# Optimization experiments

Hardware: AMD Instinct MI355X
Metric: run time of the kernel (lower is better)

## Reference

```python
import jax, jax.numpy as jnp
import numpy as np
from jax.scipy.special import logsumexp

N = 8192       # number of vectors being quantized
E_DIM = 768    # embedding dim
N_E = 1024     # codebook size per layer
SK_EPS = (0.0, 0.003, 0.003, 0.003)
SK_ITERS = 100
BETA = 1.0


def setup_inputs() -> dict:
    key = jax.random.key(0)
    ks = jax.random.split(key, 5)
    inp = {"x": jax.random.normal(ks[0], (N, E_DIM), jnp.float32)}
    for i in range(4):
        inp[f"codebook_{i}"] = jax.random.normal(ks[i + 1], (N_E, E_DIM), jnp.float32) * 0.02
    return inp


def _sq_dist(x, e):
    # squared euclidean cdist: [N, K]
    return (jnp.sum(x * x, axis=1, keepdims=True)
            + jnp.sum(e * e, axis=1)[None, :]
            - 2.0 * (x @ e.T))


def _sinkhorn_indices(d, eps, iters):
    # log-domain Sinkhorn on Q = exp(-d/eps); constants (1/K, 1/B) dropped
    # since they do not affect the final argmax assignment.
    logQ = -d / eps  # [N, K]

    def body(_, lq):
        lq = lq - logsumexp(lq, axis=0, keepdims=True)  # normalize per code over batch
        lq = lq - logsumexp(lq, axis=1, keepdims=True)  # normalize per sample over codes
        return lq

    logQ = jax.lax.fori_loop(0, iters, body, logQ)
    return jnp.argmax(logQ, axis=1)


def _vq_layer(residual, codebook, eps):
    d = _sq_dist(residual, codebook)
    if eps > 0:
        indices = _sinkhorn_indices(d, eps, SK_ITERS)
    else:
        indices = jnp.argmin(d, axis=1)
    x_q = codebook[indices]  # gather [N, E_DIM]
    sg = jax.lax.stop_gradient
    loss = jnp.mean((sg(x_q) - residual) ** 2) + BETA * jnp.mean((x_q - sg(residual)) ** 2)
    x_q = residual + sg(x_q - residual)  # straight-through estimator
    return x_q, loss, indices


def reference(x, codebook_0, codebook_1, codebook_2, codebook_3):
    codebooks = (codebook_0, codebook_1, codebook_2, codebook_3)
    residual = x
    x_q = jnp.zeros_like(x)
    losses, all_idx = [], []
    for cb, eps in zip(codebooks, SK_EPS):
        xr, loss, idx = _vq_layer(residual, cb, eps)
        residual = residual - xr
        x_q = x_q + xr
        losses.append(loss)
        all_idx.append(idx)
    mean_loss = jnp.stack(losses).mean()
    indices = jnp.stack(all_idx, axis=-1)  # [N, num_quantizers]
    return x_q, mean_loss, indices
```

## Files before the change

kernel.cpp:

```cpp
#include <hip/hip_runtime.h>
#include <math.h>

#define N_VEC   8192
#define EDIM    768
#define NCODES  1024
#define SKITERS 100
#define ROWS_PB 32
#define CHUNKS  (N_VEC / ROWS_PB)
#define DYN_LDS ((32 * NCODES + 32) * 4)

__device__ __forceinline__ void ast(float* p, float v) {
  __hip_atomic_store(p, v, __ATOMIC_RELAXED, __HIP_MEMORY_SCOPE_AGENT);
}
__device__ __forceinline__ void asti(int* p, int v) {
  __hip_atomic_store(p, v, __ATOMIC_RELAXED, __HIP_MEMORY_SCOPE_AGENT);
}
__device__ __forceinline__ int aldi(int* p) {
  return __hip_atomic_load(p, __ATOMIC_RELAXED, __HIP_MEMORY_SCOPE_AGENT);
}
union MS { unsigned long long u; float2 f; };
__device__ __forceinline__ void astms(unsigned long long* p, float m, float s) {
  MS x; x.f.x = m; x.f.y = s;
  __hip_atomic_store(p, x.u, __ATOMIC_RELAXED, __HIP_MEMORY_SCOPE_AGENT);
}
__device__ __forceinline__ float2 aldms(unsigned long long* p) {
  MS x; x.u = __hip_atomic_load(p, __ATOMIC_RELAXED, __HIP_MEMORY_SCOPE_AGENT);
  return x.f;
}
union TV { unsigned long long u; struct { float v; unsigned g; } p; };
__device__ __forceinline__ TV tvload(const unsigned long long* p) {
  TV x; x.u = __hip_atomic_load((unsigned long long*)p, __ATOMIC_RELAXED, __HIP_MEMORY_SCOPE_AGENT);
  return x;
}
__device__ __forceinline__ void tvstore(unsigned long long* p, float v, unsigned g) {
  TV x; x.p.v = v; x.p.g = g;
  __hip_atomic_store(p, x.u, __ATOMIC_RELAXED, __HIP_MEMORY_SCOPE_AGENT);
}

__device__ __forceinline__ float np_base96_sq(const float* a) {
  float r[8];
#pragma unroll
  for (int j = 0; j < 8; ++j) r[j] = __fmul_rn(a[j], a[j]);
  for (int i = 8; i < 96; i += 8) {
#pragma unroll
    for (int j = 0; j < 8; ++j) r[j] = __fadd_rn(r[j], __fmul_rn(a[i + j], a[i + j]));
  }
  float c01 = __fadd_rn(r[0], r[1]);
  float c23 = __fadd_rn(r[2], r[3]);
  float c45 = __fadd_rn(r[4], r[5]);
  float c67 = __fadd_rn(r[6], r[7]);
  return __fadd_rn(__fadd_rn(c01, c23), __fadd_rn(c45, c67));
}
__device__ __forceinline__ float np_ssq768(const float* a) {
  float L[8];
#pragma unroll
  for (int t = 0; t < 8; ++t) L[t] = np_base96_sq(a + 96 * t);
  float a01 = __fadd_rn(L[0], L[1]);
  float a23 = __fadd_rn(L[2], L[3]);
  float a45 = __fadd_rn(L[4], L[5]);
  float a67 = __fadd_rn(L[6], L[7]);
  return __fadd_rn(__fadd_rn(a01, a23), __fadd_rn(a45, a67));
}

__global__ __launch_bounds__(64) void rows_ssq(const float* __restrict__ a,
                                               float* __restrict__ out, int nrows) {
  int row = blockIdx.x * 64 + threadIdx.x;
  if (row < nrows) out[row] = np_ssq768(a + (size_t)row * EDIM);
}

#define BM 128
#define BN 128
#define BK 16
template <bool LAYER0>
__global__ __launch_bounds__(256) void gemm_d(const float* __restrict__ A,
                                              const float* __restrict__ B,
                                              const float* __restrict__ sumrr,
                                              const float* __restrict__ sumee,
                                              float* __restrict__ V) {
  __shared__ float As[BK][BM];
  __shared__ float Bs[BK][BN];
  int tid = threadIdx.x;
  int bm = blockIdx.y * BM;
  int bn = blockIdx.x * BN;
  int lr = tid >> 1;
  int lc = (tid & 1) << 3;
  const float* Ap = A + (size_t)(bm + lr) * EDIM + lc;
  const float* Bp = B + (size_t)(bn + lr) * EDIM + lc;
  float acc[8][8];
#pragma unroll
  for (int i = 0; i < 8; ++i)
#pragma unroll
    for (int j = 0; j < 8; ++j) acc[i][j] = 0.f;
  int ty = tid >> 4, tx = tid & 15;
  for (int k0 = 0; k0 < EDIM; k0 += BK) {
    float4 a0 = *(const float4*)(Ap + k0);
    float4 a1 = *(const float4*)(Ap + k0 + 4);
    float4 b0 = *(const float4*)(Bp + k0);
    float4 b1 = *(const float4*)(Bp + k0 + 4);
    __syncthreads();
    As[lc + 0][lr] = a0.x; As[lc + 1][lr] = a0.y; As[lc + 2][lr] = a0.z; As[lc + 3][lr] = a0.w;
    As[lc + 4][lr] = a1.x; As[lc + 5][lr] = a1.y; As[lc + 6][lr] = a1.z; As[lc + 7][lr] = a1.w;
    Bs[lc + 0][lr] = b0.x; Bs[lc + 1][lr] = b0.y; Bs[lc + 2][lr] = b0.z; Bs[lc + 3][lr] = b0.w;
    Bs[lc + 4][lr] = b1.x; Bs[lc + 5][lr] = b1.y; Bs[lc + 6][lr] = b1.z; Bs[lc + 7][lr] = b1.w;
    __syncthreads();
#pragma unroll
    for (int k = 0; k < BK; ++k) {
      float av[8], bv[8];
      *(float4*)(av)     = *(const float4*)(&As[k][ty * 8]);
      *(float4*)(av + 4) = *(const float4*)(&As[k][ty * 8 + 4]);
      *(float4*)(bv)     = *(const float4*)(&Bs[k][tx * 8]);
      *(float4*)(bv + 4) = *(const float4*)(&Bs[k][tx * 8 + 4]);
#pragma unroll
      for (int i = 0; i < 8; ++i)
#pragma unroll
        for (int j = 0; j < 8; ++j) acc[i][j] = __fmaf_rn(av[i], bv[j], acc[i][j]);
    }
  }
#pragma unroll
  for (int i = 0; i < 8; ++i) {
    int row = bm + ty * 8 + i;
    float srr = sumrr[row];
    float* Vp = V + (size_t)row * NCODES + bn + tx * 8;
#pragma unroll
    for (int j = 0; j < 8; ++j) {
      int col = bn + tx * 8 + j;
      float s1 = __fadd_rn(srr, sumee[col]);
      float dv = __fsub_rn(s1, __fmul_rn(2.0f, acc[i][j]));
      Vp[j] = LAYER0 ? dv : __fdiv_rn(-dv, 0.003f);
    }
  }
}

__device__ __forceinline__ void accf(float w, float& m, float& s) {
  float d = __fsub_rn(w, m);
  float e = expf(-fabsf(d));
  bool gt = (w > m);
  s = gt ? __fadd_rn(__fmul_rn(s, e), 1.0f) : __fadd_rn(s, e);
  m = gt ? w : m;
}
__device__ __forceinline__ void mergef(float mo, float so, float& m, float& s) {
  float mn = fmaxf(m, mo);
  if (mn == -INFINITY) { s = 0.f; return; }
  float d = __fsub_rn(mo, m);
  float e = expf(-fabsf(d));
  bool gt = (mo > m);
  s = gt ? __fadd_rn(__fmul_rn(s, e), so) : __fadd_rn(s, __fmul_rn(so, e));
  m = mn;
}

__global__ __launch_bounds__(1024) void sk_persist(float* __restrict__ lq,
                                                   unsigned long long* __restrict__ part,
                                                   unsigned long long* __restrict__ cT,
                                                   int* __restrict__ parr,
                                                   int* __restrict__ xarr,
                                                   unsigned gen0) {
  extern __shared__ float lds[];
  float (*vL)[NCODES] = (float(*)[NCODES])lds;
  float* rowLs = lds + 32 * NCODES;
  int tid = threadIdx.x, b = blockIdx.x;
  int wave = tid >> 6, lane = tid & 63;
  int r0 = b * ROWS_PB;

  float v[32];
#pragma unroll
  for (int r = 0; r < 32; ++r) v[r] = lq[(size_t)(r0 + r) * NCODES + tid];

#define COLCHAIN_ARRIVE(GEN)                                                  \
  do {                                                                        \
    float m = -INFINITY, s = 0.f;                                             \
    _Pragma("unroll")                                                         \
    for (int r = 0; r < 32; ++r) accf(v[r], m, s);                            \
    astms(&part[(size_t)b * NCODES + tid], m, s);                             \
    asm volatile("s_waitcnt vmcnt(0)" ::: "memory");                          \
    __syncthreads();                                                          \
    if (tid == 0) asti(&parr[b * 16], (GEN));                                 \
  } while (0)

  COLCHAIN_ARRIVE(1);

  for (int t = 0; t < SKITERS; ++t) {
    int gen = t + 1;
    unsigned cg = gen0 + (unsigned)gen;

    if (wave == 0) {
      if (b < 8) {
        if (lane < 32) {
          int* fl = &parr[(b * 32 + lane) * 16];
          while (aldi(fl) < gen) __builtin_amdgcn_s_sleep(1);
        }
        asm volatile("" ::: "memory");
        if (lane == 0) asti(&xarr[b * 16], gen);
      }
      if (lane < 8) {
        int* fl = &xarr[lane * 16];
        while (aldi(fl) < gen) __builtin_amdgcn_s_sleep(1);
      }
      asm volatile("" ::: "memory");
      float m = -INFINITY, s = 0.f;
      if (lane < 32) {
        int colj = lane >> 3, grp = lane & 7;
        int col = 4 * b + colj;
#pragma unroll
        for (int qb = 0; qb < 32; qb += 16) {
          float2 pv[16];
#pragma unroll
          for (int q = 0; q < 16; ++q)
            pv[q] = aldms(&part[(size_t)(grp * 32 + qb + q) * NCODES + col]);
#pragma unroll
          for (int q = 0; q < 16; ++q) mergef(pv[q].x, pv[q].y, m, s);
        }
      }
      float mm = -INFINITY, ss = 0.f;
#pragma unroll
      for (int g2 = 0; g2 < 8; ++g2) {
        float mo = __shfl(m, ((lane & 3) << 3) + g2, 64);
        float so = __shfl(s, ((lane & 3) << 3) + g2, 64);
        mergef(mo, so, mm, ss);
      }
      if (lane < 4) tvstore(&cT[4 * b + lane], __fadd_rn(logf(ss), mm), cg);
    }

    float cl;
    {
      TV cv = tvload(&cT[tid]);
      while (cv.p.g < cg) { __builtin_amdgcn_s_sleep(1); cv = tvload(&cT[tid]); }
      cl = cv.p.v;
    }

#pragma unroll
    for (int r = 0; r < 32; ++r) {
      v[r] = __fsub_rn(v[r], cl);
      vL[r][tid] = v[r];
    }
    __syncthreads();

#pragma unroll
    for (int rr = 0; rr < 2; ++rr) {
      int row = wave * 2 + rr;
      float vals[16];
#pragma unroll
      for (int k = 0; k < 16; ++k) vals[k] = vL[row][lane + (k << 6)];
      float mx = vals[0];
#pragma unroll
      for (int k = 1; k < 16; ++k) mx = fmaxf(mx, vals[k]);
      for (int off = 32; off; off >>= 1) mx = fmaxf(mx, __shfl_xor(mx, off, 64));
      float s = 0.f;
#pragma unroll
      for (int k = 0; k < 16; ++k) s = __fadd_rn(s, expf(__fsub_rn(vals[k], mx)));
      for (int off = 32; off; off >>= 1) s = __fadd_rn(s, __shfl_xor(s, off, 64));
      if (lane == 0) rowLs[row] = __fadd_rn(logf(s), mx);
    }
    __syncthreads();
#pragma unroll
    for (int r = 0; r < 32; ++r) v[r] = __fsub_rn(v[r], rowLs[r]);

    if (t < SKITERS - 1) COLCHAIN_ARRIVE(gen + 1);
  }

#pragma unroll
  for (int r = 0; r < 32; ++r) lq[(size_t)(r0 + r) * NCODES + tid] = v[r];
#undef COLCHAIN_ARRIVE
}

template <int MODE>
__global__ __launch_bounds__(256) void epi(const float* __restrict__ V,
                                           const float* __restrict__ rin,
                                           const float* __restrict__ cb,
                                           float* __restrict__ rout,
                                           double* __restrict__ rowssq,
                                           float* __restrict__ idx_out,
                                           int layer) {
  int i = blockIdx.x;
  int tid = threadIdx.x;
  const float* Vrow = V + (size_t)i * NCODES;
  float bv = MODE ? -INFINITY : INFINITY;
  int bj = 0;
  for (int j = tid; j < NCODES; j += 256) {
    float v = Vrow[j];
    bool better = MODE ? (v > bv) : (v < bv);
    if (better) { bv = v; bj = j; }
  }
  __shared__ float sv[256];
  __shared__ int   sj[256];
  sv[tid] = bv; sj[tid] = bj;
  __syncthreads();
  for (int st = 128; st; st >>= 1) {
    if (tid < st) {
      float v2 = sv[tid + st]; int j2 = sj[tid + st];
      bool better = MODE ? (v2 > sv[tid]) : (v2 < sv[tid]);
      if (better || (v2 == sv[tid] && j2 < sj[tid])) { sv[tid] = v2; sj[tid] = j2; }
    }
    __syncthreads();
  }
  int idx = sj[0];
  const float* crow = cb + (size_t)idx * EDIM;
  double p = 0.0;
  for (int c = tid; c < EDIM; c += 256) {
    float rn = __fsub_rn(rin[(size_t)i * EDIM + c], crow[c]);
    rout[(size_t)i * EDIM + c] = rn;
    p += (double)rn * (double)rn;
  }
  for (int off = 32; off; off >>= 1) p += __shfl_xor(p, off, 64);
  __shared__ double wsum[4];
  if ((tid & 63) == 0) wsum[tid >> 6] = p;
  __syncthreads();
  if (tid == 0) {
    rowssq[i] = wsum[0] + wsum[1] + wsum[2] + wsum[3];
    idx_out[(size_t)i * 4 + layer] = (float)idx;
  }
}

__global__ __launch_bounds__(1024) void loss_final(const double* __restrict__ rowssq,
                                                   float* __restrict__ out_loss) {
  int tid = threadIdx.x;
  __shared__ double acc[16];
  __shared__ double ltot;
  if (tid == 0) ltot = 0.0;
  __syncthreads();
  for (int l = 0; l < 4; ++l) {
    double p = 0.0;
    for (int i = tid; i < N_VEC; i += 1024) p += rowssq[l * N_VEC + i];
    for (int off = 32; off; off >>= 1) p += __shfl_xor(p, off, 64);
    if ((tid & 63) == 0) acc[tid >> 6] = p;
    __syncthreads();
    if (tid == 0) {
      double sl = 0.0;
      for (int w = 0; w < 16; ++w) sl += acc[w];
      ltot += 2.0 * sl / ((double)N_VEC * (double)EDIM);
    }
    __syncthreads();
  }
  if (tid == 0) out_loss[0] = (float)(ltot * 0.25);
}

__global__ __launch_bounds__(256) void xq_final(const float* __restrict__ x,
                                                float* __restrict__ out) {
  size_t i = ((size_t)blockIdx.x * 256 + threadIdx.x) * 4;
  float4 xv = *(const float4*)(x + i);
  float4 rv = *(const float4*)(out + i);
  float4 o;
  o.x = __fsub_rn(xv.x, rv.x); o.y = __fsub_rn(xv.y, rv.y);
  o.z = __fsub_rn(xv.z, rv.z); o.w = __fsub_rn(xv.w, rv.w);
  *(float4*)(out + i) = o;
}

extern "C" void kernel_launch(void* const* d_in, const int* in_sizes, int n_in,
                              void* d_out, int out_size, void* d_ws, size_t ws_size,
                              hipStream_t stream) {
  const float* x = (const float*)d_in[0];
  const float* cbs[4] = {(const float*)d_in[1], (const float*)d_in[2],
                         (const float*)d_in[3], (const float*)d_in[4]};
  float* out = (float*)d_out;
  float* resid = out;
  float* loss_out = out + (size_t)N_VEC * EDIM;
  float* idx_out = loss_out + 1;

  float* ws = (float*)d_ws;
  float* lq = ws;
  unsigned long long* part = (unsigned long long*)(lq + (size_t)N_VEC * NCODES);
  unsigned long long* cT = part + (size_t)CHUNKS * NCODES;
  float* sumrr = (float*)(cT + NCODES);
  float* sumee = sumrr + N_VEC;
  double* rowssq = (double*)(sumee + 4 * NCODES);
  int* flagbase = (int*)(rowssq + 4 * N_VEC);

  static int lds_set = 0;
  if (!lds_set) {
    hipFuncSetAttribute((const void*)sk_persist,
                        hipFuncAttributeMaxDynamicSharedMemorySize, DYN_LDS);
    lds_set = 1;
  }

  hipMemsetAsync(cT, 0, NCODES * 8, stream);
  hipMemsetAsync(flagbase, 0, 4 * 8192 * sizeof(int), stream);

  for (int l = 0; l < 4; ++l)
    rows_ssq<<<NCODES / 64, 64, 0, stream>>>(cbs[l], sumee + l * NCODES, NCODES);
  rows_ssq<<<N_VEC / 64, 64, 0, stream>>>(x, sumrr, N_VEC);

  for (int l = 0; l < 4; ++l) {
    const float* rin = (l == 0) ? x : resid;
    if (l == 0) {
      gemm_d<true><<<dim3(NCODES / BN, N_VEC / BM), 256, 0, stream>>>(rin, cbs[l], sumrr, sumee + l * NCODES, lq);
      epi<0><<<N_VEC, 256, 0, stream>>>(lq, rin, cbs[l], resid, rowssq + (size_t)l * N_VEC, idx_out, l);
    } else {
      gemm_d<false><<<dim3(NCODES / BN, N_VEC / BM), 256, 0, stream>>>(rin, cbs[l], sumrr, sumee + l * NCODES, lq);
      int* lf = flagbase + l * 8192;
      sk_persist<<<CHUNKS, 1024, DYN_LDS, stream>>>(lq, part, cT,
                                                    lf, lf + 4096, (unsigned)(256 * l));
      epi<1><<<N_VEC, 256, 0, stream>>>(lq, rin, cbs[l], resid, rowssq + (size_t)l * N_VEC, idx_out, l);
    }
    if (l < 3)
      rows_ssq<<<N_VEC / 64, 64, 0, stream>>>(resid, sumrr, N_VEC);
  }
  loss_final<<<1, 1024, 0, stream>>>(rowssq, loss_out);
  xq_final<<<(N_VEC * EDIM / 4) / 256, 256, 0, stream>>>(x, out);
}
```

Baseline: 6.576 ms.

## Spread column-partial reduction across eight waves with LDS handoff flags

The per-iteration column logsumexp merge now runs across waves 0-7 instead of a single wave. Each wave waits on its own xarr flag and merges 32 partials for 4 columns, then writes to LDS and sets an LDS done flag that wave 0 polls before the final merge. The parr arrival check moves to wave 8. The goal is to overlap the flag waits and global loads across waves and shorten the serial critical path of the cross-block barrier. In exchange it adds LDS spin-waiting and more waves polling global flags.

```diff
diff --git a/kernel.cpp b/kernel.cpp
--- a/kernel.cpp
+++ b/kernel.cpp
@@ -7,11 +7,8 @@
 #define SKITERS 100
 #define ROWS_PB 32
 #define CHUNKS  (N_VEC / ROWS_PB)
-#define DYN_LDS ((32 * NCODES + 32) * 4)
-
-__device__ __forceinline__ void ast(float* p, float v) {
-  __hip_atomic_store(p, v, __ATOMIC_RELAXED, __HIP_MEMORY_SCOPE_AGENT);
-}
+#define DYN_LDS ((32 * NCODES + 128) * 4)
+
 __device__ __forceinline__ void asti(int* p, int v) {
   __hip_atomic_store(p, v, __ATOMIC_RELAXED, __HIP_MEMORY_SCOPE_AGENT);
 }
@@ -157,9 +154,14 @@
   extern __shared__ float lds[];
   float (*vL)[NCODES] = (float(*)[NCODES])lds;
   float* rowLs = lds + 32 * NCODES;
+  float* mM = rowLs + 32;
+  float* sS = mM + 32;
+  volatile int* ldsdone = (volatile int*)(sS + 32);
   int tid = threadIdx.x, b = blockIdx.x;
   int wave = tid >> 6, lane = tid & 63;
   int r0 = b * ROWS_PB;
+
+  if (tid < 8) ldsdone[tid] = 0;
 
   float v[32];
 #pragma unroll
@@ -182,42 +184,55 @@
     int gen = t + 1;
     unsigned cg = gen0 + (unsigned)gen;
 
-    if (wave == 0) {
-      if (b < 8) {
-        if (lane < 32) {
-          int* fl = &parr[(b * 32 + lane) * 16];
-          while (aldi(fl) < gen) __builtin_amdgcn_s_sleep(1);
-        }
-        asm volatile("" ::: "memory");
-        if (lane == 0) asti(&xarr[b * 16], gen);
-      }
-      if (lane < 8) {
-        int* fl = &xarr[lane * 16];
+    if (b < 8 && wave == 8) {
+      if (lane < 32) {
+        int* fl = &parr[(b * 32 + lane) * 16];
         while (aldi(fl) < gen) __builtin_amdgcn_s_sleep(1);
       }
       asm volatile("" ::: "memory");
-      float m = -INFINITY, s = 0.f;
-      if (lane < 32) {
-        int colj = lane >> 3, grp = lane & 7;
-        int col = 4 * b + colj;
+      if (lane == 0) asti(&xarr[b * 16], gen);
+    }
+
+    if (wave < 8) {
+      {
+        int* fl = &xarr[wave * 16];
+        while (aldi(fl) < gen) __builtin_amdgcn_s_sleep(1);
+      }
+      asm volatile("" ::: "memory");
+      if (lane < 4) {
+        int col = 4 * b + lane;
+        float m = -INFINITY, s = 0.f;
 #pragma unroll
         for (int qb = 0; qb < 32; qb += 16) {
           float2 pv[16];
 #pragma unroll
           for (int q = 0; q < 16; ++q)
-            pv[q] = aldms(&part[(size_t)(grp * 32 + qb + q) * NCODES + col]);
+            pv[q] = aldms(&part[(size_t)(wave * 32 + qb + q) * NCODES + col]);
 #pragma unroll
           for (int q = 0; q < 16; ++q) mergef(pv[q].x, pv[q].y, m, s);
         }
+        mM[wave * 4 + lane] = m;
+        sS[wave * 4 + lane] = s;
       }
-      float mm = -INFINITY, ss = 0.f;
-#pragma unroll
-      for (int g2 = 0; g2 < 8; ++g2) {
-        float mo = __shfl(m, ((lane & 3) << 3) + g2, 64);
-        float so = __shfl(s, ((lane & 3) << 3) + g2, 64);
-        mergef(mo, so, mm, ss);
+      asm volatile("s_waitcnt lgkmcnt(0)" ::: "memory");
+      if (lane == 0) ldsdone[wave] = gen;
+    }
+
+    if (wave == 0) {
+      for (;;) {
+        int ok = 1;
+        if (lane < 8) ok = (ldsdone[lane] >= gen);
+        if (__all(ok)) break;
+        __builtin_amdgcn_s_sleep(1);
       }
-      if (lane < 4) tvstore(&cT[4 * b + lane], __fadd_rn(logf(ss), mm), cg);
+      asm volatile("" ::: "memory");
+      if (lane < 4) {
+        float mm = -INFINITY, ss = 0.f;
+#pragma unroll
+        for (int g2 = 0; g2 < 8; ++g2)
+          mergef(mM[g2 * 4 + lane], sS[g2 * 4 + lane], mm, ss);
+        tvstore(&cT[4 * b + lane], __fadd_rn(logf(ss), mm), cg);
+      }
     }
 
     float cl;
```

New measurement: 7.374 ms. +12.1%, slower.
